# Kernel tuning notes

Hardware: AMD Instinct MI355X
Metric: run time of the kernel (lower is better)

The kernel has to match this reference:

```python
import jax, jax.numpy as jnp
import numpy as np

NUM_ATOM_TYPE = 120
NUM_BOND_TYPE = 6
NUM_LAYER = 5
EMB_DIM = 300
N_NODES = 50000
N_EDGES = 800000
BN_EPS = 1e-5


def setup_inputs() -> dict:
    key = jax.random.key(0)
    ks = jax.random.split(key, 12)
    x = jax.random.randint(ks[0], (N_NODES, 2), 0, NUM_ATOM_TYPE, dtype=jnp.int32)
    edge_index = jax.random.randint(ks[1], (2, N_EDGES), 0, N_NODES, dtype=jnp.int32)
    edge_attr = jax.random.randint(ks[2], (N_EDGES, 2), 0, 3, dtype=jnp.int32)
    s = 1.0 / np.sqrt(EMB_DIM)
    x_emb = jax.random.uniform(ks[3], (NUM_ATOM_TYPE, EMB_DIM), minval=-s, maxval=s, dtype=jnp.float32)
    edge_emb = jax.random.uniform(ks[4], (NUM_LAYER, NUM_BOND_TYPE, EMB_DIM), minval=-s, maxval=s, dtype=jnp.float32)
    W1 = jax.random.normal(ks[5], (NUM_LAYER, EMB_DIM, 2 * EMB_DIM), dtype=jnp.float32) * s
    b1 = jnp.zeros((NUM_LAYER, 2 * EMB_DIM), dtype=jnp.float32)
    W2 = jax.random.normal(ks[6], (NUM_LAYER, 2 * EMB_DIM, EMB_DIM), dtype=jnp.float32) * (1.0 / np.sqrt(2 * EMB_DIM))
    b2 = jnp.zeros((NUM_LAYER, EMB_DIM), dtype=jnp.float32)
    bn_gamma = jnp.ones((NUM_LAYER, EMB_DIM), dtype=jnp.float32)
    bn_beta = jnp.zeros((NUM_LAYER, EMB_DIM), dtype=jnp.float32)
    return {"x": x, "edge_index": edge_index, "edge_attr": edge_attr,
            "x_emb": x_emb, "edge_emb": edge_emb,
            "W1": W1, "b1": b1, "W2": W2, "b2": b2,
            "bn_gamma": bn_gamma, "bn_beta": bn_beta}


def _forward(x, edge_index, edge_attr, x_emb, edge_emb, W1, b1, W2, b2, bn_gamma, bn_beta):
    n = x.shape[0]
    # node embedding: sum of x_embedding1 over feature columns (faithful to source)
    h = x_emb[x[:, 0]] + x_emb[x[:, 1]]  # [N, D]
    # add self loops once (same for every layer)
    loop = jnp.arange(n, dtype=edge_index.dtype)
    src = jnp.concatenate([edge_index[0], loop])  # [E+N]
    dst = jnp.concatenate([edge_index[1], loop])
    # self-loop edge_attr: zeros with column 0 = 4
    sl = jnp.zeros((n, edge_attr.shape[1]), dtype=edge_attr.dtype).at[:, 0].set(4)
    ea = jnp.concatenate([edge_attr, sl], axis=0)  # [E+N, 2]
    for layer in range(NUM_LAYER):
        # edge embeddings: sum of edge_embedding1 over attr columns (faithful)
        ee = edge_emb[layer][ea[:, 0]] + edge_emb[layer][ea[:, 1]]  # [E+N, D]
        msg = h[src] + ee
        agg = jax.ops.segment_sum(msg, dst, num_segments=n)  # scatter-add
        # GIN MLP (classification branch applies mlp to aggregate only)
        hid = jax.nn.relu(agg @ W1[layer] + b1[layer])
        h = hid @ W2[layer] + b2[layer]
        # BatchNorm1d, training-mode batch statistics
        mu = jnp.mean(h, axis=0)
        var = jnp.var(h, axis=0)
        h = (h - mu) * jax.lax.rsqrt(var + BN_EPS) * bn_gamma[layer] + bn_beta[layer]
        if layer != NUM_LAYER - 1:
            h = jax.nn.relu(h)
        # dropout ratio is 0 -> no-op
    return h  # JK == 'last'


def reference(x, edge_index, edge_attr, x_emb, edge_emb, W1, b1, W2, b2, bn_gamma, bn_beta):
    return _forward(x, edge_index, edge_attr, x_emb, edge_emb, W1, b1, W2, b2, bn_gamma, bn_beta)
```

## Files before the change

kernel.cpp:

```cpp
#include <hip/hip_runtime.h>
#include <hip/hip_bf16.h>

typedef unsigned short u16;
typedef _Float16 f16;
typedef f16 f16x8 __attribute__((ext_vector_type(8)));
typedef f16 half2t __attribute__((ext_vector_type(2)));
typedef u16 u16x8 __attribute__((ext_vector_type(8)));
typedef float f32x4 __attribute__((ext_vector_type(4)));

#define NN 50000
#define NE 800000
#define D  300
#define DP 320
#define HP 640
#define MT 32
#define NROWPAD 50048

__device__ __forceinline__ float h2f(u16 u){ f16 h = __builtin_bit_cast(f16, u); return (float)h; }
__device__ __forceinline__ u16 f2h(float f){ f16 h = (f16)f; return __builtin_bit_cast(u16, h); }
__device__ __forceinline__ float hlo(unsigned u){ half2t h = __builtin_bit_cast(half2t, u); return (float)h.x; }
__device__ __forceinline__ float hhi(unsigned u){ half2t h = __builtin_bit_cast(half2t, u); return (float)h.y; }
__device__ __forceinline__ unsigned packh(float x, float y){ half2t h; h.x = (f16)x; h.y = (f16)y; return __builtin_bit_cast(unsigned, h); }

__device__ __forceinline__ void gl_lds16(const void* g, void* l){
  __builtin_amdgcn_global_load_lds((const __attribute__((address_space(1))) unsigned int*)g,
                                   (__attribute__((address_space(3))) unsigned int*)l, 16, 0, 0);
}

__device__ __forceinline__ f32x4 mfma_f16(u16x8 a, u16x8 b, f32x4 c){
  return __builtin_amdgcn_mfma_f32_16x16x32_f16(__builtin_bit_cast(f16x8, a),
                                                __builtin_bit_cast(f16x8, b), c, 0, 0, 0);
}

__global__ void k_count(const int* __restrict__ ei, const int* __restrict__ ea,
                        int* __restrict__ cnt, int* __restrict__ ccnt){
  int e = blockIdx.x * 256 + threadIdx.x;
  if (e < NE){
    int d = ei[NE + e];
    atomicAdd(&cnt[d], 1);
    int t = ea[2*e] * 3 + ea[2*e + 1];
    atomicAdd(&ccnt[d * 12 + t], 1);
  }
}

__global__ void k_scan1(const int* __restrict__ cnt, int* __restrict__ rp, int* __restrict__ bsum){
  __shared__ int s[1024];
  int i = blockIdx.x * 1024 + threadIdx.x;
  int v = (i < NN) ? cnt[i] : 0;
  s[threadIdx.x] = v;
  __syncthreads();
  for (int off = 1; off < 1024; off <<= 1){
    int t = (threadIdx.x >= off) ? s[threadIdx.x - off] : 0;
    __syncthreads();
    s[threadIdx.x] += t;
    __syncthreads();
  }
  if (i < NN) rp[i] = s[threadIdx.x] - v;
  if (threadIdx.x == 1023) bsum[blockIdx.x] = s[1023];
}

__global__ void k_scan2(int* __restrict__ bsum, int nb){
  __shared__ int s[64];
  int v = (threadIdx.x < nb) ? bsum[threadIdx.x] : 0;
  s[threadIdx.x] = v; __syncthreads();
  for (int off = 1; off < 64; off <<= 1){
    int t = (threadIdx.x >= off) ? s[threadIdx.x - off] : 0;
    __syncthreads();
    s[threadIdx.x] += t;
    __syncthreads();
  }
  if (threadIdx.x < nb) bsum[threadIdx.x] = s[threadIdx.x] - v;
}

__global__ void k_scan3(int* __restrict__ rp, int* __restrict__ cur, const int* __restrict__ bsum){
  int i = blockIdx.x * 256 + threadIdx.x;
  if (i < NN){ int v = rp[i] + bsum[i >> 10]; rp[i] = v; cur[i] = v; }
  if (i == 0) rp[NN] = NE;
}

__global__ void k_fill(const int* __restrict__ ei, int* __restrict__ cur, int* __restrict__ pack){
  int e = blockIdx.x * 256 + threadIdx.x;
  if (e >= NE) return;
  int d = ei[NE + e];
  int pos = atomicAdd(&cur[d], 1);
  pack[pos] = ei[e];
}

__global__ void k_wconv(const float* __restrict__ W1, const float* __restrict__ W2,
                        u16* __restrict__ W1t, u16* __restrict__ W2t){
  int i = blockIdx.x * 256 + threadIdx.x;
  {
    int l = i / (HP * DP); int rem = i % (HP * DP); int n = rem / DP, k = rem % DP;
    float v = (n < 600 && k < D) ? W1[((size_t)l * D + k) * 600 + n] : 0.f;
    W1t[i] = f2h(v);
  }
  {
    int l = i / (DP * HP); int rem = i % (DP * HP); int n = rem / HP, k = rem % HP;
    float v = (n < D && k < 600) ? W2[((size_t)l * 600 + k) * D + n] : 0.f;
    W2t[i] = f2h(v);
  }
}

__global__ void k_nodeemb(const int* __restrict__ x, const float* __restrict__ xemb, u16* __restrict__ hb){
  int v = blockIdx.x, c = threadIdx.x;
  float y = 0.f;
  if (c < D){
    int a = x[2*v], b = x[2*v + 1];
    y = xemb[(size_t)a * D + c] + xemb[(size_t)b * D + c];
  }
  hb[(size_t)v * DP + c] = f2h(y);
}

__global__ __launch_bounds__(256) void k_agg(const u16* __restrict__ hb, const int* __restrict__ rp,
    const int* __restrict__ pack, const int* __restrict__ ccnt,
    const float* __restrict__ eemb, u16* __restrict__ agg){
  __shared__ float se[4 * DP];
  for (int i = threadIdx.x; i < 4 * DP; i += 256){
    int t = i / DP, c = i % DP;
    int row = (t == 3) ? 4 : t;
    se[i] = (c < D) ? eemb[row * D + c] : 0.f;
  }
  __syncthreads();
  const int wid = threadIdx.x >> 6, lane = threadIdx.x & 63;
  const int v = blockIdx.x * 4 + wid;
  if (v >= NN) return;
  const char* __restrict__ hbb = (const char*)hb;
  const unsigned lo8 = (unsigned)lane * 8u;
  const unsigned lo4 = 512u + (unsigned)lane * 4u;
  float a0, a1, a2, a3, a4 = 0.f, a5 = 0.f;
  {
    unsigned off = (unsigned)v * 640u;
    uint2 u = *(const uint2*)(hbb + off + lo8);
    a0 = hlo(u.x); a1 = hhi(u.x); a2 = hlo(u.y); a3 = hhi(u.y);
    if (lane < 32){ unsigned uw = *(const unsigned*)(hbb + off + lo4); a4 = hlo(uw); a5 = hhi(uw); }
  }
  int p = rp[v];
  const int pe = rp[v + 1];
  for (; p + 2 <= pe; p += 2){
    unsigned off0 = (unsigned)pack[p] * 640u;
    unsigned off1 = (unsigned)pack[p + 1] * 640u;
    uint2 u0 = *(const uint2*)(hbb + off0 + lo8);
    uint2 u1 = *(const uint2*)(hbb + off1 + lo8);
    unsigned w0v = 0, w1v = 0;
    if (lane < 32){
      w0v = *(const unsigned*)(hbb + off0 + lo4);
      w1v = *(const unsigned*)(hbb + off1 + lo4);
    }
    a0 += hlo(u0.x) + hlo(u1.x);
    a1 += hhi(u0.x) + hhi(u1.x);
    a2 += hlo(u0.y) + hlo(u1.y);
    a3 += hhi(u0.y) + hhi(u1.y);
    a4 += hlo(w0v) + hlo(w1v);
    a5 += hhi(w0v) + hhi(w1v);
  }
  if (p < pe){
    unsigned off0 = (unsigned)pack[p] * 640u;
    uint2 u0 = *(const uint2*)(hbb + off0 + lo8);
    a0 += hlo(u0.x); a1 += hhi(u0.x); a2 += hlo(u0.y); a3 += hhi(u0.y);
    if (lane < 32){ unsigned w0v = *(const unsigned*)(hbb + off0 + lo4); a4 += hlo(w0v); a5 += hhi(w0v); }
  }
  const int* cc = ccnt + (size_t)v * 12;
  int4 cA = *(const int4*)cc;
  int4 cB = *(const int4*)(cc + 4);
  int c8 = cc[8];
  float w0f = (float)(2 * cA.x + cA.y + cA.z + cA.w + cB.z + 1);
  float w1f = (float)(cA.y + cA.w + 2 * cB.x + cB.y + cB.w);
  float w2f = (float)(cA.z + cB.y + cB.z + cB.w + 2 * c8);
  {
    const float4 e0v = *(const float4*)&se[0 * DP + 4 * lane];
    const float4 e1v = *(const float4*)&se[1 * DP + 4 * lane];
    const float4 e2v = *(const float4*)&se[2 * DP + 4 * lane];
    const float4 e4v = *(const float4*)&se[3 * DP + 4 * lane];
    a0 += w0f * e0v.x + w1f * e1v.x + w2f * e2v.x + e4v.x;
    a1 += w0f * e0v.y + w1f * e1v.y + w2f * e2v.y + e4v.y;
    a2 += w0f * e0v.z + w1f * e1v.z + w2f * e2v.z + e4v.z;
    a3 += w0f * e0v.w + w1f * e1v.w + w2f * e2v.w + e4v.w;
  }
  char* ab = (char*)agg;
  unsigned oo = (unsigned)v * 640u;
  uint2 st; st.x = packh(a0, a1); st.y = packh(a2, a3);
  *(uint2*)(ab + oo + lo8) = st;
  if (lane < 32){
    int cI = 256 + 2 * lane;
    a4 += w0f * se[0 * DP + cI]     + w1f * se[1 * DP + cI]     + w2f * se[2 * DP + cI]     + se[3 * DP + cI];
    a5 += w0f * se[0 * DP + cI + 1] + w1f * se[1 * DP + cI + 1] + w2f * se[2 * DP + cI + 1] + se[3 * DP + cI + 1];
    *(unsigned*)(ab + oo + lo4) = packh(a4, a5);
  }
}

__global__ __launch_bounds__(512) void k_mlp(const u16* __restrict__ agg,
    const u16* __restrict__ W1t, const u16* __restrict__ W2t,
    const float* __restrict__ b1, const float* __restrict__ b2,
    float* __restrict__ h2, float* __restrict__ sums){
  __shared__ __attribute__((aligned(16))) u16 hid[MT * 320];
  __shared__ __attribute__((aligned(16))) u16 stA[MT * 32];
  __shared__ __attribute__((aligned(16))) u16 stB[320 * 32];
  const int tid = threadIdx.x;
  const int lane = tid & 63, w = tid >> 6;
  const int mh = w >> 2, nq = w & 3;
  const int r0 = blockIdx.x * MT;
  const int l15 = lane & 15;
  const unsigned kb16 = ((unsigned)(lane >> 4)) * 16u;
  f32x4 accB[5] = {};
  for (int h = 0; h < 2; ++h){
    f32x4 accA[5] = {};
    for (int ks = 0; ks < 10; ++ks){
      __syncthreads();
      #pragma unroll
      for (int i = 0; i < 3; ++i){
        const int cbase = i * 512 + w * 64;
        if (cbase < 128){
          const int c = cbase + lane;
          gl_lds16(agg + (size_t)(r0 + (c >> 2)) * DP + ks * 32 + (c & 3) * 8,
                   stA + cbase * 8);
        } else if (cbase < 1408){
          const int c = cbase - 128 + lane;
          gl_lds16(W1t + (size_t)(h * 320 + (c >> 2)) * DP + ks * 32 + (c & 3) * 8,
                   stB + (cbase - 128) * 8);
        }
      }
      asm volatile("s_waitcnt vmcnt(0)" ::: "memory");
      __syncthreads();
      u16x8 af = *(const u16x8*)&stA[(mh * 16 + l15) * 32 + (lane >> 4) * 8];
      u16x8 bf[5];
      #pragma unroll
      for (int n = 0; n < 5; ++n)
        bf[n] = *(const u16x8*)&stB[(nq * 80 + n * 16 + l15) * 32 + (lane >> 4) * 8];
      #pragma unroll
      for (int n = 0; n < 5; ++n) accA[n] = mfma_f16(af, bf[n], accA[n]);
    }
    #pragma unroll
    for (int n = 0; n < 5; ++n){
      const int colL = nq * 80 + n * 16 + l15;
      const int colG = h * 320 + colL;
      const float bv = (colG < 600) ? b1[colG] : 0.f;
      #pragma unroll
      for (int r = 0; r < 4; ++r){
        const unsigned row = (unsigned)(mh * 16) + ((unsigned)(lane >> 4)) * 4u + (unsigned)r;
        const float vv = fmaxf(accA[n][r] + bv, 0.f);
        const unsigned byte = row * 640u + ((2u * (unsigned)colL) ^ ((row & 7u) << 4));
        *(u16*)((char*)hid + byte) = f2h(vv);
      }
    }
    for (int ks = 0; ks < 10; ++ks){
      __syncthreads();
      #pragma unroll
      for (int i = 0; i < 3; ++i){
        const int cbase = i * 512 + w * 64;
        if (cbase < 1280){
          const int c = cbase + lane;
          gl_lds16(W2t + (size_t)(c >> 2) * HP + (h * 10 + ks) * 32 + (c & 3) * 8,
                   stB + cbase * 8);
        }
      }
      asm volatile("s_waitcnt vmcnt(0)" ::: "memory");
      __syncthreads();
      const unsigned arow = (unsigned)(mh * 16 + l15);
      const unsigned abyte = arow * 640u + (((unsigned)ks * 64u + kb16) ^ ((arow & 7u) << 4));
      u16x8 af = *(const u16x8*)((const char*)hid + abyte);
      u16x8 bf[5];
      #pragma unroll
      for (int n = 0; n < 5; ++n)
        bf[n] = *(const u16x8*)&stB[(nq * 80 + n * 16 + l15) * 32 + (lane >> 4) * 8];
      #pragma unroll
      for (int n = 0; n < 5; ++n) accB[n] = mfma_f16(af, bf[n], accB[n]);
    }
  }
  float sn[5] = {0,0,0,0,0}, qn[5] = {0,0,0,0,0};
  const int row0 = r0 + mh * 16 + (lane >> 4) * 4;
  #pragma unroll
  for (int n = 0; n < 5; ++n){
    const int col = nq * 80 + n * 16 + l15;
    if (col >= D) continue;
    const float bv = b2[col];
    #pragma unroll
    for (int r = 0; r < 4; ++r){
      const int row = row0 + r;
      if (row < NN){
        const float vv = accB[n][r] + bv;
        h2[(size_t)row * D + col] = vv;
        sn[n] += vv; qn[n] += vv * vv;
      }
    }
  }
  #pragma unroll
  for (int n = 0; n < 5; ++n){
    const int col = nq * 80 + n * 16 + l15;
    float s = sn[n], q = qn[n];
    s += __shfl_xor(s, 16); q += __shfl_xor(q, 16);
    s += __shfl_xor(s, 32); q += __shfl_xor(q, 32);
    if (col < D && (lane >> 4) == 0){
      atomicAdd(&sums[col], s);
      atomicAdd(&sums[DP + col], q);
    }
  }
}

template<bool LAST>
__global__ void k_bnapply(const float* h2, const float* __restrict__ sums,
    const float* __restrict__ gamma, const float* __restrict__ beta,
    u16* __restrict__ hb, float* outp){
  int r = blockIdx.x, c = threadIdx.x;
  float y = 0.f;
  if (c < D){
    float mu  = sums[c] * (1.f / NN);
    float var = sums[DP + c] * (1.f / NN) - mu * mu;
    float x = h2[(size_t)r * D + c];
    float s = var + 1e-5f;
    float inv = rsqrtf(s);
    inv = inv * (1.5f - 0.5f * s * inv * inv);
    y = (x - mu) * inv * gamma[c] + beta[c];
    if (!LAST) y = fmaxf(y, 0.f);
  }
  if (LAST){ if (c < D) outp[(size_t)r * D + c] = y; }
  else hb[(size_t)r * DP + c] = f2h(y);
}

extern "C" void kernel_launch(void* const* d_in, const int* in_sizes, int n_in,
                              void* d_out, int out_size, void* d_ws, size_t ws_size,
                              hipStream_t stream){
  (void)in_sizes; (void)n_in; (void)out_size; (void)ws_size;
  const int*   x    = (const int*)d_in[0];
  const int*   ei   = (const int*)d_in[1];
  const int*   ea   = (const int*)d_in[2];
  const float* xemb = (const float*)d_in[3];
  const float* eemb = (const float*)d_in[4];
  const float* W1   = (const float*)d_in[5];
  const float* b1   = (const float*)d_in[6];
  const float* W2   = (const float*)d_in[7];
  const float* b2   = (const float*)d_in[8];
  const float* gam  = (const float*)d_in[9];
  const float* bet  = (const float*)d_in[10];
  float* out = (float*)d_out;

  char* w = (char*)d_ws;
  size_t off = 0;
  auto alloc = [&](size_t b){ void* p = w + off; off += (b + 255) & ~(size_t)255; return p; };
  u16* hb    = (u16*)alloc((size_t)NROWPAD * DP * 2);
  u16* aggb  = (u16*)alloc((size_t)NROWPAD * DP * 2);
  u16* W1t   = (u16*)alloc((size_t)5 * HP * DP * 2);
  u16* W2t   = (u16*)alloc((size_t)5 * DP * HP * 2);
  int* rp    = (int*)alloc((NN + 1) * 4);
  int* cnt   = (int*)alloc((size_t)NN * 4);
  int* cur   = (int*)alloc((size_t)NN * 4);
  int* bsum  = (int*)alloc(64 * 4);
  int* pack  = (int*)alloc((size_t)NE * 4);
  int* ccnt  = (int*)alloc((size_t)NN * 12 * 4);
  float* sums5 = (float*)alloc(5 * 2 * DP * 4);
  float* h2  = out;

  hipMemsetAsync(cnt, 0, NN * 4, stream);
  hipMemsetAsync(ccnt, 0, (size_t)NN * 12 * 4, stream);
  hipMemsetAsync(sums5, 0, 5 * 2 * DP * 4, stream);
  k_count<<<NE / 256, 256, 0, stream>>>(ei, ea, cnt, ccnt);
  k_scan1<<<(NN + 1023) / 1024, 1024, 0, stream>>>(cnt, rp, bsum);
  k_scan2<<<1, 64, 0, stream>>>(bsum, (NN + 1023) / 1024);
  k_scan3<<<(NN + 255) / 256, 256, 0, stream>>>(rp, cur, bsum);
  k_fill<<<NE / 256, 256, 0, stream>>>(ei, cur, pack);
  k_wconv<<<(5 * HP * DP) / 256, 256, 0, stream>>>(W1, W2, W1t, W2t);
  k_nodeemb<<<NN, DP, 0, stream>>>(x, xemb, hb);

  for (int l = 0; l < 5; ++l){
    float* sums = sums5 + l * 2 * DP;
    k_agg<<<(NN + 3) / 4, 256, 0, stream>>>(hb, rp, pack, ccnt, eemb + (size_t)l * 6 * D, aggb);
    k_mlp<<<NROWPAD / MT, 512, 0, stream>>>(aggb,
        W1t + (size_t)l * HP * DP, W2t + (size_t)l * DP * HP,
        b1 + l * 600, b2 + l * D, h2, sums);
    if (l < 4) k_bnapply<false><<<NN, DP, 0, stream>>>(h2, sums, gam + l * D, bet + l * D, hb, nullptr);
    else       k_bnapply<true ><<<NN, DP, 0, stream>>>(h2, sums, gam + l * D, bet + l * D, nullptr, out);
  }
}
```

Before: 1.697 ms.

## Double-buffer weight tiles and preload the full aggregate tile in the MLP kernel

The fused MLP kernel now loads the block's whole 32-row aggregate tile into LDS once, instead of reloading a 32-column slice at every k-step. The W1/W2 weight slices go through a two-slot LDS buffer: the next stage is issued before computing on the current one, and the wait is relaxed from vmcnt(0) to vmcnt(3). This aims to overlap global-to-LDS transfers with the MFMA work and drop one barrier-plus-full-drain per step. In exchange, LDS use grows to about 80KB per block, which can reduce how many blocks fit on each CU.

```diff
diff --git a/kernel.cpp b/kernel.cpp
--- a/kernel.cpp
+++ b/kernel.cpp
@@ -192,42 +192,69 @@
     const u16* __restrict__ W1t, const u16* __restrict__ W2t,
     const float* __restrict__ b1, const float* __restrict__ b2,
     float* __restrict__ h2, float* __restrict__ sums){
-  __shared__ __attribute__((aligned(16))) u16 hid[MT * 320];
-  __shared__ __attribute__((aligned(16))) u16 stA[MT * 32];
-  __shared__ __attribute__((aligned(16))) u16 stB[320 * 32];
+  __shared__ __attribute__((aligned(16))) u16 stAfull[1280 * 8];
+  __shared__ __attribute__((aligned(16))) u16 stBuf[2 * 1280 * 8];
+  __shared__ __attribute__((aligned(16))) u16 hid[MT * DP];
   const int tid = threadIdx.x;
   const int lane = tid & 63, w = tid >> 6;
   const int mh = w >> 2, nq = w & 3;
   const int r0 = blockIdx.x * MT;
   const int l15 = lane & 15;
   const unsigned kb16 = ((unsigned)(lane >> 4)) * 16u;
+
+  const int j0 = w, j1 = w + 8, j2 = (w < 4) ? (w + 16) : w;
+  const int c0 = j0 * 64 + lane, c1 = j1 * 64 + lane, c2 = j2 * 64 + lane;
+  const int r_0 = c0 % 320, k_0 = c0 / 320;
+  const int r_1 = c1 % 320, k_1 = c1 / 320;
+  const int r_2 = c2 % 320, k_2 = c2 / 320;
+  const int s1_0 = r_0 * DP + k_0 * 8, s1_1 = r_1 * DP + k_1 * 8, s1_2 = r_2 * DP + k_2 * 8;
+  const int s2_0 = r_0 * HP + k_0 * 8, s2_1 = r_1 * HP + k_1 * 8, s2_2 = r_2 * HP + k_2 * 8;
+  const int d0 = j0 * 512, d1 = j1 * 512, d2 = j2 * 512;
+
+  auto STAGE = [&](int sn){
+    u16* db = stBuf + ((sn & 1) ? 1280 * 8 : 0);
+    const int hh = sn / 20, pp = (sn % 20) / 10, kk = sn % 10;
+    if (pp == 0){
+      const u16* sp = W1t + hh * (320 * DP) + kk * 32;
+      gl_lds16(sp + s1_0, db + d0);
+      gl_lds16(sp + s1_1, db + d1);
+      gl_lds16(sp + s1_2, db + d2);
+    } else {
+      const u16* sp = W2t + hh * 320 + kk * 32;
+      gl_lds16(sp + s2_0, db + d0);
+      gl_lds16(sp + s2_1, db + d1);
+      gl_lds16(sp + s2_2, db + d2);
+    }
+  };
+
+  {
+    const int cA0 = j0 * 64 + lane, cA1 = j1 * 64 + lane;
+    gl_lds16(agg + (size_t)(r0 + (cA0 & 31)) * DP + (cA0 >> 5) * 8, stAfull + j0 * 512);
+    gl_lds16(agg + (size_t)(r0 + (cA1 & 31)) * DP + (cA1 >> 5) * 8, stAfull + j1 * 512);
+    if (w < 4){
+      const int cA2 = (w + 16) * 64 + lane;
+      gl_lds16(agg + (size_t)(r0 + (cA2 & 31)) * DP + (cA2 >> 5) * 8, stAfull + (w + 16) * 512);
+    }
+  }
+  STAGE(0);
+
   f32x4 accB[5] = {};
+  int s = 0;
   for (int h = 0; h < 2; ++h){
     f32x4 accA[5] = {};
-    for (int ks = 0; ks < 10; ++ks){
+    for (int ks = 0; ks < 10; ++ks, ++s){
+      STAGE(s + 1);
+      asm volatile("s_waitcnt vmcnt(3)" ::: "memory");
       __syncthreads();
-      #pragma unroll
-      for (int i = 0; i < 3; ++i){
-        const int cbase = i * 512 + w * 64;
-        if (cbase < 128){
-          const int c = cbase + lane;
-          gl_lds16(agg + (size_t)(r0 + (c >> 2)) * DP + ks * 32 + (c & 3) * 8,
-                   stA + cbase * 8);
-        } else if (cbase < 1408){
-          const int c = cbase - 128 + lane;
-          gl_lds16(W1t + (size_t)(h * 320 + (c >> 2)) * DP + ks * 32 + (c & 3) * 8,
-                   stB + (cbase - 128) * 8);
-        }
-      }
-      asm volatile("s_waitcnt vmcnt(0)" ::: "memory");
+      const u16* rb = stBuf + ((s & 1) ? 1280 * 8 : 0);
+      u16x8 af = *(const u16x8*)&stAfull[((ks * 4 + (lane >> 4)) * 32 + mh * 16 + l15) * 8];
+      u16x8 bf[5];
+      #pragma unroll
+      for (int n = 0; n < 5; ++n)
+        bf[n] = *(const u16x8*)&rb[((lane >> 4) * 320 + nq * 80 + n * 16 + l15) * 8];
+      #pragma unroll
+      for (int n = 0; n < 5; ++n) accA[n] = mfma_f16(af, bf[n], accA[n]);
       __syncthreads();
-      u16x8 af = *(const u16x8*)&stA[(mh * 16 + l15) * 32 + (lane >> 4) * 8];
-      u16x8 bf[5];
-      #pragma unroll
-      for (int n = 0; n < 5; ++n)
-        bf[n] = *(const u16x8*)&stB[(nq * 80 + n * 16 + l15) * 32 + (lane >> 4) * 8];
-      #pragma unroll
-      for (int n = 0; n < 5; ++n) accA[n] = mfma_f16(af, bf[n], accA[n]);
     }
     #pragma unroll
     for (int n = 0; n < 5; ++n){
@@ -242,28 +269,25 @@
         *(u16*)((char*)hid + byte) = f2h(vv);
       }
     }
-    for (int ks = 0; ks < 10; ++ks){
+    for (int ks = 0; ks < 10; ++ks, ++s){
+      if (s < 39){
+        STAGE(s + 1);
+        asm volatile("s_waitcnt vmcnt(3)" ::: "memory");
+      } else {
+        asm volatile("s_waitcnt vmcnt(0)" ::: "memory");
+      }
       __syncthreads();
-      #pragma unroll
-      for (int i = 0; i < 3; ++i){
-        const int cbase = i * 512 + w * 64;
-        if (cbase < 1280){
-          const int c = cbase + lane;
-          gl_lds16(W2t + (size_t)(c >> 2) * HP + (h * 10 + ks) * 32 + (c & 3) * 8,
-                   stB + cbase * 8);
-        }
-      }
-      asm volatile("s_waitcnt vmcnt(0)" ::: "memory");
-      __syncthreads();
+      const u16* rb = stBuf + ((s & 1) ? 1280 * 8 : 0);
       const unsigned arow = (unsigned)(mh * 16 + l15);
       const unsigned abyte = arow * 640u + (((unsigned)ks * 64u + kb16) ^ ((arow & 7u) << 4));
       u16x8 af = *(const u16x8*)((const char*)hid + abyte);
       u16x8 bf[5];
       #pragma unroll
       for (int n = 0; n < 5; ++n)
-        bf[n] = *(const u16x8*)&stB[(nq * 80 + n * 16 + l15) * 32 + (lane >> 4) * 8];
+        bf[n] = *(const u16x8*)&rb[((lane >> 4) * 320 + nq * 80 + n * 16 + l15) * 8];
       #pragma unroll
       for (int n = 0; n < 5; ++n) accB[n] = mfma_f16(af, bf[n], accB[n]);
+      __syncthreads();
     }
   }
   float sn[5] = {0,0,0,0,0}, qn[5] = {0,0,0,0,0};
@@ -286,12 +310,12 @@
   #pragma unroll
   for (int n = 0; n < 5; ++n){
     const int col = nq * 80 + n * 16 + l15;
-    float s = sn[n], q = qn[n];
-    s += __shfl_xor(s, 16); q += __shfl_xor(q, 16);
-    s += __shfl_xor(s, 32); q += __shfl_xor(q, 32);
+    float sv = sn[n], qv = qn[n];
+    sv += __shfl_xor(sv, 16); qv += __shfl_xor(qv, 16);
+    sv += __shfl_xor(sv, 32); qv += __shfl_xor(qv, 32);
     if (col < D && (lane >> 4) == 0){
-      atomicAdd(&sums[col], s);
-      atomicAdd(&sums[DP + col], q);
+      atomicAdd(&sums[col], sv);
+      atomicAdd(&sums[DP + col], qv);
     }
   }
 }
```

After: 2.301 ms. 35.6% more time.
